# Optimization experiments

Measured on AMD Instinct MI355X. Metric: run time of the kernel, lower is better.

The kernel has to match this reference:

```python
import jax, jax.numpy as jnp
import numpy as np

N_LAYERS = 2
NUM_BRANCHES = 3
TOPK_START = 10
TOPK_END = 3


def normalize_adj(adj):
    # symmetric degree normalization: D^-1/2 (A + I) D^-1/2
    n = adj.shape[0]
    a = jnp.clip(adj + jnp.eye(n, dtype=adj.dtype), 1e-8, jnp.inf)
    row_sum = jnp.clip(a.sum(axis=1), 1e-8, jnp.inf)
    d = jnp.clip(row_sum ** -0.5, 0.0, 100.0)
    return d[:, None] * a * d[None, :]


def setup_inputs() -> dict:
    key = jax.random.key(0)
    k1, k2 = jax.random.split(key)
    B, T, N, C = 512, 16, 22, 64
    x = jax.random.normal(k1, (B, T, N, C), dtype=jnp.float32)
    # emulate nn.Parameter init: clamp(adj,0,1)*0.01 + 0.05*I
    raw = jax.random.uniform(k2, (N, N), dtype=jnp.float32)
    adj = jnp.clip(raw, 0.0, 1.0) * 0.01 + 0.05 * jnp.eye(N, dtype=jnp.float32)
    branch_temps = jnp.ones((NUM_BRANCHES,), dtype=jnp.float32)
    fusion_logits = jnp.zeros((N_LAYERS, NUM_BRANCHES), dtype=jnp.float32)
    return {"x": x, "adj": adj, "branch_temps": branch_temps, "fusion_logits": fusion_logits}


def reference(x, adj, branch_temps, fusion_logits):
    B, T, N, C = x.shape
    # [B, T, N, C] -> [B, N, T*C]
    x0 = jnp.transpose(x, (0, 2, 1, 3)).reshape(B, N, T * C)
    A = normalize_adj(jnp.clip(adj, 0.0, 1.0))          # [N, N]
    temps = jnp.clip(branch_temps, 0.1, 10.0)           # [nb]
    eye = jnp.eye(N, dtype=x0.dtype)

    xb = x0
    for layer in range(N_LAYERS):
        K = int(TOPK_START - (TOPK_START - TOPK_END) * (layer / max(1, N_LAYERS - 1)))
        K = min(K, N)
        alpha = jax.nn.softmax(fusion_logits[layer])    # [nb]
        # cosine similarity, masked by normalized adjacency
        xn = xb / (jnp.linalg.norm(xb, axis=-1, keepdims=True) + 1e-6)
        sim = jnp.einsum('bnd,bmd->bnm', xn, xn) * A    # [B, N, N]
        # per-branch temperature + diagonal boost
        att = sim[None] / temps[:, None, None, None] + 0.1 * eye  # [nb, B, N, N]
        # annealed top-k sparsification (zeros still participate in softmax, as in torch)
        _, idx = jax.lax.top_k(att, K)                  # [nb, B, N, K]
        mask = jax.nn.one_hot(idx, N, dtype=att.dtype).sum(axis=-2)  # [nb, B, N, N]
        att = jax.nn.softmax(att * mask, axis=-1)
        y = jnp.einsum('kbnm,bmd->kbnd', att, xb)       # branch aggregation
        xb = jnp.einsum('k,kbnd->bnd', alpha, y)        # fusion
        if layer > 0:
            xb = xb + x0
        if layer < N_LAYERS - 1:
            xb = jax.nn.relu(xb)  # dropout identity in eval mode
    return xb, A
```

## Files before the change

kernel.cpp:

```cpp
#include <hip/hip_runtime.h>
#include <hip/hip_bf16.h>

#define BATCH  512
#define TT     16
#define NN     22
#define CC     64
#define DD     1024
#define NB     3
#define NTHR   512
#define WPAD   40

typedef __bf16 bf16x8 __attribute__((ext_vector_type(8)));
typedef float  f32x4  __attribute__((ext_vector_type(4)));
typedef float  f32x16 __attribute__((ext_vector_type(16)));

__device__ __forceinline__ unsigned bf16rne(float x) {
  unsigned u = __float_as_uint(x);
  u += 0x7fffu + ((u >> 16) & 1u);
  return u >> 16;
}
__device__ __forceinline__ unsigned pack2(float a, float b) {
  return bf16rne(a) | (bf16rne(b) << 16);
}
__device__ __forceinline__ unsigned xoff(unsigned m, unsigned d) {
  return ((d >> 4) * 6u + (m >> 2)) * 64u + (m & 3u) * 16u + (d & 15u);
}

__global__ __launch_bounds__(NTHR) void mbdsca_fused(
    const float* __restrict__ x,
    const float* __restrict__ adj,
    const float* __restrict__ btemps,
    const float* __restrict__ flogits,
    float* __restrict__ out)
{
  __shared__ unsigned short xs[6 * 64 * 64];
  __shared__ float As[NN][NN];
  __shared__ float Gp[4][NN][NN];
  __shared__ unsigned short Wh[32][WPAD];
  __shared__ unsigned short Wl[32][WPAD];
  __shared__ float deg[NN];
  __shared__ float alphas[2][NB];
  __shared__ float tvals[NB];

  const int tid  = threadIdx.x;
  const int b    = blockIdx.x;
  const int lane = tid & 63;
  const int wv   = tid >> 6;
  const float* __restrict__ xb0 = x + (size_t)b * (TT * NN * CC);

  float4 xv[11];
  #pragma unroll
  for (int j = 0; j < 11; ++j)
    xv[j] = *(const float4*)(&xb0[(size_t)(tid + j * NTHR) * 4]);

  if (tid < NN * NN) {
    int n = tid / NN, m = tid - n * NN;
    float v = adj[tid];
    v = fminf(fmaxf(v, 0.0f), 1.0f);
    if (n == m) v += 1.0f;
    As[n][m] = fmaxf(v, 1e-8f);
  }
  if (tid < NB) tvals[tid] = fminf(fmaxf(btemps[tid], 0.1f), 10.0f);
  for (int i = tid; i < 32 * WPAD / 2; i += NTHR) {
    ((unsigned*)Wh)[i] = 0u;
    ((unsigned*)Wl)[i] = 0u;
  }
  __syncthreads();

  if (tid < NN) {
    float s = 0.0f;
    for (int m = 0; m < NN; ++m) s += As[tid][m];
    s = fmaxf(s, 1e-8f);
    deg[tid] = fminf(fmaxf(1.0f / sqrtf(s), 0.0f), 100.0f);
  }
  if (tid == 0) {
    for (int l = 0; l < 2; ++l) {
      float l0 = flogits[l*NB+0], l1 = flogits[l*NB+1], l2 = flogits[l*NB+2];
      float mx = fmaxf(l0, fmaxf(l1, l2));
      float e0 = __expf(l0-mx), e1 = __expf(l1-mx), e2 = __expf(l2-mx);
      float s = e0 + e1 + e2;
      alphas[l][0] = e0/s; alphas[l][1] = e1/s; alphas[l][2] = e2/s;
    }
  }
  __syncthreads();

  if (tid < NN * NN) {
    int n = tid / NN, m = tid - n * NN;
    As[n][m] = deg[n] * As[n][m] * deg[m];
  }
  #pragma unroll
  for (int j = 0; j < 11; ++j) {
    int f4  = tid + j * NTHR;
    int t   = f4 / (NN * (CC/4));
    int rem = f4 - t * (NN * (CC/4));
    int n   = rem >> 4;
    int c4  = rem & 15;
    uint2 p; p.x = pack2(xv[j].x, xv[j].y); p.y = pack2(xv[j].z, xv[j].w);
    *(uint2*)(&xs[xoff(n, t * 64 + c4 * 4)]) = p;
  }
  {
    int m  = 22 + (tid >> 8);
    int d0 = (tid & 255) * 4;
    *(uint2*)(&xs[xoff(m, d0)]) = make_uint2(0u, 0u);
  }
  __syncthreads();

  const unsigned xsb = (unsigned)(unsigned long long)(void*)&xs[0];

  for (int layer = 0; layer < 2; ++layer) {
    const int K = (layer == 0) ? 10 : 3;

    if (wv < 4) {
      int row = lane & 31; if (row > NN-1) row = NN-1;
      const int hi = lane >> 5;
      f32x16 acc0 = {}, acc1 = {};
      __builtin_amdgcn_s_setprio(1);
      #pragma unroll
      for (int s = 0; s < 16; ++s) {
        int d0 = (wv * 16 + s) * 16 + hi * 8;
        bf16x8 a = *(const bf16x8*)(&xs[xoff(row, d0)]);
        if (s & 1) acc1 = __builtin_amdgcn_mfma_f32_32x32x16_bf16(a, a, acc1, 0, 0, 0);
        else       acc0 = __builtin_amdgcn_mfma_f32_32x32x16_bf16(a, a, acc0, 0, 0, 0);
      }
      __builtin_amdgcn_s_setprio(0);
      #pragma unroll
      for (int r = 0; r < 16; ++r) {
        float vv = acc0[r] + acc1[r];
        int orow = (r & 3) + 8 * (r >> 2) + 4 * hi;
        int ocol = lane & 31;
        if (orow < NN && ocol < NN) Gp[wv][orow][ocol] = vv;
      }
    }
    __syncthreads();

    {
      const int j    = lane & 31;
      const int base = lane & 32;
      const float t0 = tvals[0], t1 = tvals[1], t2 = tvals[2];
      const float a0 = alphas[layer][0], a1 = alphas[layer][1], a2 = alphas[layer][2];
      #pragma unroll
      for (int pass = 0; pass < 2; ++pass) {
        const int n = wv * 2 + (lane >> 5) + pass * 16;
        if (n < NN) {
          const bool valid = (j < NN);
          const int  jj    = valid ? j : 0;
          float g   = Gp[0][n][jj] + Gp[1][n][jj] + Gp[2][n][jj] + Gp[3][n][jj];
          float gjj = Gp[0][jj][jj] + Gp[1][jj][jj] + Gp[2][jj][jj] + Gp[3][jj][jj];
          float gnn = Gp[0][n][n]  + Gp[1][n][n]  + Gp[2][n][n]  + Gp[3][n][n];
          float dj = 1.0f / (sqrtf(gjj) + 1e-6f);
          float dn = 1.0f / (sqrtf(gnn) + 1e-6f);
          float v  = g * dn * dj * As[n][jj];
          if (!valid) v = 0.0f;
          float vnn = __shfl(v, base + n);
          float vh0 = vnn + 0.1f * t0;
          float vh1 = vnn + 0.1f * t1;
          float vh2 = vnn + 0.1f * t2;
          int rank = 0, c0 = 0, c1 = 0, c2 = 0;
          #pragma unroll
          for (int i = 0; i < NN; ++i) {
            float vi = __shfl(v, base + i);
            if (i != n) {
              rank += ((vi > v)   || (vi == v   && i < j)) ? 1 : 0;
              c0   += ((vi > vh0) || (vi == vh0 && i < n)) ? 1 : 0;
              c1   += ((vi > vh1) || (vi == vh1 && i < n)) ? 1 : 0;
              c2   += ((vi > vh2) || (vi == vh2 && i < n)) ? 1 : 0;
            }
          }
          float w = 0.0f;
          #pragma unroll
          for (int k = 0; k < NB; ++k) {
            const float vh  = (k == 0) ? vh0 : (k == 1) ? vh1 : vh2;
            const int   cd  = (k == 0) ? c0  : (k == 1) ? c1  : c2;
            const float tk  = (k == 0) ? t0  : (k == 1) ? t1  : t2;
            const float ak  = (k == 0) ? a0  : (k == 1) ? a1  : a2;
            const float rtk = 1.0f / tk;
            bool dgt = (vh > v) || (vh == v && n < j);
            int  rk  = (j == n) ? cd : (rank + (dgt ? 1 : 0));
            bool sel = (rk < K) && valid;
            float att = sel ? (((j == n) ? vh : v) * rtk) : 0.0f;
            float mx = att;
            mx = fmaxf(mx, __shfl_xor(mx, 1));
            mx = fmaxf(mx, __shfl_xor(mx, 2));
            mx = fmaxf(mx, __shfl_xor(mx, 4));
            mx = fmaxf(mx, __shfl_xor(mx, 8));
            mx = fmaxf(mx, __shfl_xor(mx, 16));
            mx = fmaxf(mx, 0.0f);
            float e = valid ? __expf(att - mx) : 0.0f;
            float s = e;
            s += __shfl_xor(s, 1);
            s += __shfl_xor(s, 2);
            s += __shfl_xor(s, 4);
            s += __shfl_xor(s, 8);
            s += __shfl_xor(s, 16);
            w += e * (ak / s);
          }
          if (valid) {
            unsigned h = bf16rne(w);
            Wh[n][j] = (unsigned short)h;
            Wl[n][j] = (unsigned short)bf16rne(w - __uint_as_float(h << 16));
          }
        }
      }
    }
    __syncthreads();

    {
      const int n_b = lane & 31;
      const int ko  = (lane >> 5) * 8;
      bf16x8 w0h = *(const bf16x8*)(&Wh[n_b][ko]);
      bf16x8 w0l = *(const bf16x8*)(&Wl[n_b][ko]);
      bf16x8 w1h = *(const bf16x8*)(&Wh[n_b][16 + ko]);
      bf16x8 w1l = *(const bf16x8*)(&Wl[n_b][16 + ko]);
      const int dpr     = lane & 31;
      const int dsub_in = dpr >> 4;
      const int dcol    = dpr & 15;
      const int hi5     = lane >> 5;
      unsigned mqA  = (unsigned)(hi5 * 2);
      unsigned mqB0 = 4 + mqA;  if (mqB0 > 5) mqB0 = 5;
      unsigned mqB1 = 5 + mqA;  if (mqB1 > 5) mqB1 = 5;
      #pragma unroll
      for (int g = 0; g < 2; ++g) {
        const int dt0 = wv * 4 + g * 2;
        const int dt1 = dt0 + 1;
        const unsigned rb0 = xsb + (unsigned)(dt0 * 2 + dsub_in) * 768u + (unsigned)dcol * 8u;
        const unsigned rb1 = xsb + (unsigned)(dt1 * 2 + dsub_in) * 768u + (unsigned)dcol * 8u;
        unsigned long long s00, s01, s02, s03, s10, s11, s12, s13;
        asm volatile("ds_read_b64_tr_b16 %0, %1" : "=v"(s00) : "v"(rb0 + mqA * 128u));
        asm volatile("ds_read_b64_tr_b16 %0, %1" : "=v"(s01) : "v"(rb0 + (mqA + 1u) * 128u));
        asm volatile("ds_read_b64_tr_b16 %0, %1" : "=v"(s02) : "v"(rb0 + mqB0 * 128u));
        asm volatile("ds_read_b64_tr_b16 %0, %1" : "=v"(s03) : "v"(rb0 + mqB1 * 128u));
        asm volatile("ds_read_b64_tr_b16 %0, %1" : "=v"(s10) : "v"(rb1 + mqA * 128u));
        asm volatile("ds_read_b64_tr_b16 %0, %1" : "=v"(s11) : "v"(rb1 + (mqA + 1u) * 128u));
        asm volatile("ds_read_b64_tr_b16 %0, %1" : "=v"(s12) : "v"(rb1 + mqB0 * 128u));
        asm volatile("ds_read_b64_tr_b16 %0, %1" : "=v"(s13) : "v"(rb1 + mqB1 * 128u));
        asm volatile("s_waitcnt lgkmcnt(0)" ::: "memory");
        __builtin_amdgcn_sched_barrier(0);
        int4 a00 = make_int4((int)s00, (int)(s00 >> 32), (int)s01, (int)(s01 >> 32));
        int4 a01 = make_int4((int)s02, (int)(s02 >> 32), (int)s03, (int)(s03 >> 32));
        int4 a10 = make_int4((int)s10, (int)(s10 >> 32), (int)s11, (int)(s11 >> 32));
        int4 a11 = make_int4((int)s12, (int)(s12 >> 32), (int)s13, (int)(s13 >> 32));
        bf16x8 A00 = __builtin_bit_cast(bf16x8, a00);
        bf16x8 A01 = __builtin_bit_cast(bf16x8, a01);
        bf16x8 A10 = __builtin_bit_cast(bf16x8, a10);
        bf16x8 A11 = __builtin_bit_cast(bf16x8, a11);
        f32x16 acc0 = {}, acc1 = {};
        __builtin_amdgcn_s_setprio(1);
        acc0 = __builtin_amdgcn_mfma_f32_32x32x16_bf16(A00, w0h, acc0, 0, 0, 0);
        acc1 = __builtin_amdgcn_mfma_f32_32x32x16_bf16(A10, w0h, acc1, 0, 0, 0);
        acc0 = __builtin_amdgcn_mfma_f32_32x32x16_bf16(A00, w0l, acc0, 0, 0, 0);
        acc1 = __builtin_amdgcn_mfma_f32_32x32x16_bf16(A10, w0l, acc1, 0, 0, 0);
        acc0 = __builtin_amdgcn_mfma_f32_32x32x16_bf16(A01, w1h, acc0, 0, 0, 0);
        acc1 = __builtin_amdgcn_mfma_f32_32x32x16_bf16(A11, w1h, acc1, 0, 0, 0);
        acc0 = __builtin_amdgcn_mfma_f32_32x32x16_bf16(A01, w1l, acc0, 0, 0, 0);
        acc1 = __builtin_amdgcn_mfma_f32_32x32x16_bf16(A11, w1l, acc1, 0, 0, 0);
        __builtin_amdgcn_s_setprio(0);
        if (n_b < NN) {
          if (layer == 0) {
            #pragma unroll
            for (int q = 0; q < 4; ++q) {
              int dqa = dt0 * 32 + 4 * hi5 + 8 * q;
              int dqb = dt1 * 32 + 4 * hi5 + 8 * q;
              uint2 pa, pb;
              pa.x = pack2(fmaxf(acc0[4*q+0], 0.f), fmaxf(acc0[4*q+1], 0.f));
              pa.y = pack2(fmaxf(acc0[4*q+2], 0.f), fmaxf(acc0[4*q+3], 0.f));
              pb.x = pack2(fmaxf(acc1[4*q+0], 0.f), fmaxf(acc1[4*q+1], 0.f));
              pb.y = pack2(fmaxf(acc1[4*q+2], 0.f), fmaxf(acc1[4*q+3], 0.f));
              *(uint2*)(&xs[xoff(n_b, dqa)]) = pa;
              *(uint2*)(&xs[xoff(n_b, dqb)]) = pb;
            }
          } else {
            #pragma unroll
            for (int q = 0; q < 4; ++q) {
              int dqa = dt0 * 32 + 4 * hi5 + 8 * q;
              int dqb = dt1 * 32 + 4 * hi5 + 8 * q;
              const float4 ra = *(const float4*)(&xb0[((dqa >> 6) * NN + n_b) * CC + (dqa & 63)]);
              const float4 rb = *(const float4*)(&xb0[((dqb >> 6) * NN + n_b) * CC + (dqb & 63)]);
              *(float4*)(&out[((size_t)b * NN + n_b) * DD + dqa]) =
                  make_float4(acc0[4*q+0] + ra.x, acc0[4*q+1] + ra.y,
                              acc0[4*q+2] + ra.z, acc0[4*q+3] + ra.w);
              *(float4*)(&out[((size_t)b * NN + n_b) * DD + dqb]) =
                  make_float4(acc1[4*q+0] + rb.x, acc1[4*q+1] + rb.y,
                              acc1[4*q+2] + rb.z, acc1[4*q+3] + rb.w);
            }
          }
        }
      }
    }
    __syncthreads();
  }

  if (b == 0 && tid < NN * NN) {
    out[(size_t)BATCH * NN * DD + tid] = As[tid / NN][tid - (tid / NN) * NN];
  }
}

extern "C" void kernel_launch(void* const* d_in, const int* in_sizes, int n_in,
                              void* d_out, int out_size, void* d_ws, size_t ws_size,
                              hipStream_t stream) {
  const float* x       = (const float*)d_in[0];
  const float* adj     = (const float*)d_in[1];
  const float* btemps  = (const float*)d_in[2];
  const float* flogits = (const float*)d_in[3];
  float* out = (float*)d_out;
  mbdsca_fused<<<BATCH, NTHR, 0, stream>>>(x, adj, btemps, flogits, out);
}
```

Baseline: 63.44 us.

## Spread Gram MFMA across all waves and parallelize top-k softmax per element

The Gram matrix computation is split across all 8 waves instead of 4, with partial results combined by shared-memory atomicAdd into one G matrix. The per-row top-k and softmax stage is restructured to one thread per (n,m) element, with per-row denominators accumulated by atomics, replacing the previous wave-shuffle reductions. The x prefetch into registers is also dropped in favour of loading directly at conversion time. This adds extra barriers and LDS atomics, and gives up the early global load overlap, in exchange for more parallel MFMA work and fewer shuffles.

```diff
diff --git a/kernel.cpp b/kernel.cpp
--- a/kernel.cpp
+++ b/kernel.cpp
@@ -35,7 +35,10 @@
 {
   __shared__ unsigned short xs[6 * 64 * 64];
   __shared__ float As[NN][NN];
-  __shared__ float Gp[4][NN][NN];
+  __shared__ float G[NN][NN];
+  __shared__ float simS[NN][NN];
+  __shared__ float attB[NB][NN][NN];
+  __shared__ float denom[NB][NN];
   __shared__ unsigned short Wh[32][WPAD];
   __shared__ unsigned short Wl[32][WPAD];
   __shared__ float deg[NN];
@@ -47,11 +50,6 @@
   const int lane = tid & 63;
   const int wv   = tid >> 6;
   const float* __restrict__ xb0 = x + (size_t)b * (TT * NN * CC);
-
-  float4 xv[11];
-  #pragma unroll
-  for (int j = 0; j < 11; ++j)
-    xv[j] = *(const float4*)(&xb0[(size_t)(tid + j * NTHR) * 4]);
 
   if (tid < NN * NN) {
     int n = tid / NN, m = tid - n * NN;
@@ -59,8 +57,10 @@
     v = fminf(fmaxf(v, 0.0f), 1.0f);
     if (n == m) v += 1.0f;
     As[n][m] = fmaxf(v, 1e-8f);
+    ((float*)G)[tid] = 0.0f;
   }
   if (tid < NB) tvals[tid] = fminf(fmaxf(btemps[tid], 0.1f), 10.0f);
+  if (tid < NB * NN) ((float*)denom)[tid] = 0.0f;
   for (int i = tid; i < 32 * WPAD / 2; i += NTHR) {
     ((unsigned*)Wh)[i] = 0u;
     ((unsigned*)Wl)[i] = 0u;
@@ -95,7 +95,8 @@
     int rem = f4 - t * (NN * (CC/4));
     int n   = rem >> 4;
     int c4  = rem & 15;
-    uint2 p; p.x = pack2(xv[j].x, xv[j].y); p.y = pack2(xv[j].z, xv[j].w);
+    const float4 v = *(const float4*)(&xb0[(size_t)f4 * 4]);
+    uint2 p; p.x = pack2(v.x, v.y); p.y = pack2(v.z, v.w);
     *(uint2*)(&xs[xoff(n, t * 64 + c4 * 4)]) = p;
   }
   {
@@ -110,14 +111,14 @@
   for (int layer = 0; layer < 2; ++layer) {
     const int K = (layer == 0) ? 10 : 3;
 
-    if (wv < 4) {
+    {
       int row = lane & 31; if (row > NN-1) row = NN-1;
       const int hi = lane >> 5;
       f32x16 acc0 = {}, acc1 = {};
       __builtin_amdgcn_s_setprio(1);
       #pragma unroll
-      for (int s = 0; s < 16; ++s) {
-        int d0 = (wv * 16 + s) * 16 + hi * 8;
+      for (int s = 0; s < 8; ++s) {
+        int d0 = (wv * 8 + s) * 16 + hi * 8;
         bf16x8 a = *(const bf16x8*)(&xs[xoff(row, d0)]);
         if (s & 1) acc1 = __builtin_amdgcn_mfma_f32_32x32x16_bf16(a, a, acc1, 0, 0, 0);
         else       acc0 = __builtin_amdgcn_mfma_f32_32x32x16_bf16(a, a, acc0, 0, 0, 0);
@@ -128,79 +129,84 @@
         float vv = acc0[r] + acc1[r];
         int orow = (r & 3) + 8 * (r >> 2) + 4 * hi;
         int ocol = lane & 31;
-        if (orow < NN && ocol < NN) Gp[wv][orow][ocol] = vv;
-      }
-    }
-    __syncthreads();
-
-    {
-      const int j    = lane & 31;
-      const int base = lane & 32;
+        if (orow < NN && ocol < NN) atomicAdd(&G[orow][ocol], vv);
+      }
+    }
+    __syncthreads();
+
+    if (tid < NN * NN) {
+      int n = tid / NN, m = tid - n * NN;
+      float g  = G[n][m];
+      float rn = 1.0f / (sqrtf(G[n][n]) + 1e-6f);
+      float rm = 1.0f / (sqrtf(G[m][m]) + 1e-6f);
+      simS[n][m] = g * rn * rm * As[n][m];
+    }
+    __syncthreads();
+
+    if (tid < NN * NN) {
+      const int n = tid / NN, m = tid - n * NN;
+      float simrow[NN];
+      #pragma unroll
+      for (int jj = 0; jj < NN / 2; ++jj) {
+        float2 pr = *(const float2*)(&simS[n][2 * jj]);
+        simrow[2 * jj]     = pr.x;
+        simrow[2 * jj + 1] = pr.y;
+      }
+      float simn = 0.f, v = 0.f, rmax_ex = -1e30f;
+      #pragma unroll
+      for (int j = 0; j < NN; ++j) {
+        float s = simrow[j];
+        simn = (j == n) ? s : simn;
+        v    = (j == m) ? s : v;
+        rmax_ex = (j == n) ? rmax_ex : fmaxf(rmax_ex, s);
+      }
       const float t0 = tvals[0], t1 = tvals[1], t2 = tvals[2];
-      const float a0 = alphas[layer][0], a1 = alphas[layer][1], a2 = alphas[layer][2];
-      #pragma unroll
-      for (int pass = 0; pass < 2; ++pass) {
-        const int n = wv * 2 + (lane >> 5) + pass * 16;
-        if (n < NN) {
-          const bool valid = (j < NN);
-          const int  jj    = valid ? j : 0;
-          float g   = Gp[0][n][jj] + Gp[1][n][jj] + Gp[2][n][jj] + Gp[3][n][jj];
-          float gjj = Gp[0][jj][jj] + Gp[1][jj][jj] + Gp[2][jj][jj] + Gp[3][jj][jj];
-          float gnn = Gp[0][n][n]  + Gp[1][n][n]  + Gp[2][n][n]  + Gp[3][n][n];
-          float dj = 1.0f / (sqrtf(gjj) + 1e-6f);
-          float dn = 1.0f / (sqrtf(gnn) + 1e-6f);
-          float v  = g * dn * dj * As[n][jj];
-          if (!valid) v = 0.0f;
-          float vnn = __shfl(v, base + n);
-          float vh0 = vnn + 0.1f * t0;
-          float vh1 = vnn + 0.1f * t1;
-          float vh2 = vnn + 0.1f * t2;
-          int rank = 0, c0 = 0, c1 = 0, c2 = 0;
-          #pragma unroll
-          for (int i = 0; i < NN; ++i) {
-            float vi = __shfl(v, base + i);
-            if (i != n) {
-              rank += ((vi > v)   || (vi == v   && i < j)) ? 1 : 0;
-              c0   += ((vi > vh0) || (vi == vh0 && i < n)) ? 1 : 0;
-              c1   += ((vi > vh1) || (vi == vh1 && i < n)) ? 1 : 0;
-              c2   += ((vi > vh2) || (vi == vh2 && i < n)) ? 1 : 0;
-            }
-          }
-          float w = 0.0f;
-          #pragma unroll
-          for (int k = 0; k < NB; ++k) {
-            const float vh  = (k == 0) ? vh0 : (k == 1) ? vh1 : vh2;
-            const int   cd  = (k == 0) ? c0  : (k == 1) ? c1  : c2;
-            const float tk  = (k == 0) ? t0  : (k == 1) ? t1  : t2;
-            const float ak  = (k == 0) ? a0  : (k == 1) ? a1  : a2;
-            const float rtk = 1.0f / tk;
-            bool dgt = (vh > v) || (vh == v && n < j);
-            int  rk  = (j == n) ? cd : (rank + (dgt ? 1 : 0));
-            bool sel = (rk < K) && valid;
-            float att = sel ? (((j == n) ? vh : v) * rtk) : 0.0f;
-            float mx = att;
-            mx = fmaxf(mx, __shfl_xor(mx, 1));
-            mx = fmaxf(mx, __shfl_xor(mx, 2));
-            mx = fmaxf(mx, __shfl_xor(mx, 4));
-            mx = fmaxf(mx, __shfl_xor(mx, 8));
-            mx = fmaxf(mx, __shfl_xor(mx, 16));
-            mx = fmaxf(mx, 0.0f);
-            float e = valid ? __expf(att - mx) : 0.0f;
-            float s = e;
-            s += __shfl_xor(s, 1);
-            s += __shfl_xor(s, 2);
-            s += __shfl_xor(s, 4);
-            s += __shfl_xor(s, 8);
-            s += __shfl_xor(s, 16);
-            w += e * (ak / s);
-          }
-          if (valid) {
-            unsigned h = bf16rne(w);
-            Wh[n][j] = (unsigned short)h;
-            Wl[n][j] = (unsigned short)bf16rne(w - __uint_as_float(h << 16));
-          }
+      const float vh0 = simn + 0.1f * t0;
+      const float vh1 = simn + 0.1f * t1;
+      const float vh2 = simn + 0.1f * t2;
+      int cnt = 0, c0 = 0, c1 = 0, c2 = 0;
+      #pragma unroll
+      for (int j = 0; j < NN; ++j) {
+        if (j == n) continue;
+        float vj = simrow[j];
+        cnt += ((vj > v)   || (vj == v   && j < m)) ? 1 : 0;
+        c0  += ((vj > vh0) || (vj == vh0 && j < n)) ? 1 : 0;
+        c1  += ((vj > vh1) || (vj == vh1 && j < n)) ? 1 : 0;
+        c2  += ((vj > vh2) || (vj == vh2 && j < n)) ? 1 : 0;
+      }
+      #pragma unroll
+      for (int k = 0; k < NB; ++k) {
+        const float vh  = (k == 0) ? vh0 : (k == 1) ? vh1 : vh2;
+        const int   cd  = (k == 0) ? c0  : (k == 1) ? c1  : c2;
+        const float tk  = (k == 0) ? t0  : (k == 1) ? t1  : t2;
+        const float rtk = 1.0f / tk;
+        int rk;
+        float own_t;
+        if (m == n) { rk = cd; own_t = vh; }
+        else {
+          bool dgt = (vh > v) || (vh == v && n < m);
+          rk = cnt + (dgt ? 1 : 0);
+          own_t = v;
         }
-      }
+        const bool sel = (rk < K);
+        const float mxf  = fmaxf(fmaxf(rmax_ex, vh) * rtk, 0.0f);
+        const float aown = sel ? own_t * rtk : 0.0f;
+        const float e = __expf(aown - mxf);
+        attB[k][n][m] = e;
+        atomicAdd(&denom[k][n], e);
+      }
+    }
+    __syncthreads();
+
+    if (tid < NN * NN) {
+      int n = tid / NN, m = tid - n * NN;
+      float w = attB[0][n][m] * (alphas[layer][0] / denom[0][n])
+              + attB[1][n][m] * (alphas[layer][1] / denom[1][n])
+              + attB[2][n][m] * (alphas[layer][2] / denom[2][n]);
+      unsigned h = bf16rne(w);
+      Wh[n][m] = (unsigned short)h;
+      Wl[n][m] = (unsigned short)bf16rne(w - __uint_as_float(h << 16));
+      ((float*)G)[tid] = 0.0f;
     }
     __syncthreads();
 
@@ -286,6 +292,7 @@
         }
       }
     }
+    if (tid < NB * NN) ((float*)denom)[tid] = 0.0f;
     __syncthreads();
   }
 
```

Result: slower. 80.99 us (+27.7%).
